# Kernel tuning notes

Hardware: AMD Instinct MI355X
Metric: run time of the kernel (lower is better)

The kernel has to match this reference:

```python
import math
import jax, jax.numpy as jnp
from jax import lax
import numpy as np

THETA = 10.0      # spiking threshold
TAU_SR = 10.0     # SRM (psp) alpha-kernel time constant
TAU_REF = 1.0     # refractory alpha-kernel time constant
SCALE_REF = 2.0   # refractory scale (kernel = -scaleRef*theta*alpha)
TAU_RHO = 1.0     # surrogate-gradient width
TS = 1.0          # simulation time step


def _alpha_filter_scan(x, tau, extra_input_fn=None):
    """Causal convolution along last (time) axis with alpha kernel
    k[n] = (n*Ts/tau) * exp(1 - n*Ts/tau)  (k[0] = 0),
    implemented exactly as a 2-state linear recurrence.
    x: [N, C, T] -> out: [N, C, T]."""
    d = jnp.float32(math.exp(-TS / tau))
    c = jnp.float32(math.e * TS / tau)
    xT = jnp.moveaxis(x, -1, 0)  # [T, N, C]

    def step(carry, xt):
        p, a = carry
        a = d * (a + p)          # alpha response from inputs up to t-1
        p = d * p + xt           # pure exponential state
        return (p, a), a * c

    z = jnp.zeros_like(xT[0])
    _, out = lax.scan(step, (z, z), xT)
    return jnp.moveaxis(out, 0, -1)


def psp(x):
    return _alpha_filter_scan(x, TAU_SR)


@jax.custom_vjp
def spike_fn(v):
    # Heaviside threshold on (membrane - theta)
    return (v >= 0).astype(v.dtype)

def _spike_fwd(v):
    return spike_fn(v), v

def _spike_bwd(v, g):
    # SLAYER surrogate gradient: exponential pdf around threshold
    grad = (1.0 / TAU_RHO) * jnp.exp(-jnp.abs(v) / TAU_RHO)
    return (g * grad,)

spike_fn.defvjp(_spike_fwd, _spike_bwd)


def spike_layer(u_in):
    """Threshold-and-refract over time. u_in: [N, C, T] psp potentials.
    Refractory response = -scaleRef*theta * alpha_{tauRef}(past spikes)."""
    d = jnp.float32(math.exp(-TS / TAU_REF))
    c = jnp.float32(math.e * TS / TAU_REF)
    ref_scale = jnp.float32(-SCALE_REF * THETA)
    uT = jnp.moveaxis(u_in, -1, 0)  # [T, N, C]

    def step(carry, ut):
        p, a = carry
        a = d * (a + p)                      # refractory potential at t
        u = ut + c * a                       # membrane potential
        s = spike_fn(u - THETA)              # spikes (0/1)
        p = d * p + ref_scale * s            # inject refractory impulse
        return (p, a), s

    z = jnp.zeros_like(uT[0])
    _, s = lax.scan(step, (z, z), uT)
    return jnp.moveaxis(s, 0, -1)


def setup_inputs() -> dict:
    key = jax.random.key(0)
    k1, k2, k3 = jax.random.split(key, 3)
    N, I, H, O, T = 64, 256, 1024, 18, 500
    # Bernoulli(0.1) input spikes
    spike_input = (jax.random.uniform(k1, (N, I, T)) < 0.1).astype(jnp.float32)
    W1 = jax.random.normal(k2, (H, I), dtype=jnp.float32) * (1.0 / math.sqrt(I))
    W2 = jax.random.normal(k3, (O, H), dtype=jnp.float32) * (1.0 / math.sqrt(H))
    return {"spike_input": spike_input, "W1": W1, "W2": W2}


def reference(spike_input, W1, W2):
    # layer 1: dense (per-timestep linear) -> psp -> spike
    y1 = jnp.einsum('nit,hi->nht', spike_input, W1)
    s1 = spike_layer(psp(y1))
    # layer 2
    y2 = jnp.einsum('nht,oh->not', s1, W2)
    s2 = spike_layer(psp(y2))
    return s2
```

## Files before the change

### kernel.cpp

```cpp
#include <hip/hip_runtime.h>


#define NN 64
#define II 256
#define HH 1024
#define OO 18
#define TT 500

#define D_SR 0.9048374180359595f
#define C_SR 0.27182818284590454f
#define D_RF 0.36787944117144233f
#define C_RF 2.718281828459045f
#define THETA 10.0f
#define REFS (-20.0f)

typedef _Float16 f16;
typedef _Float16 f16x8 __attribute__((ext_vector_type(8)));
typedef float f32x4 __attribute__((ext_vector_type(4)));

__device__ __forceinline__ void gl2lds16(const void* g, void* l) {
    __builtin_amdgcn_global_load_lds(
        (const __attribute__((address_space(1))) void*)g,
        (__attribute__((address_space(3))) void*)l, 16, 0, 0);
}

__launch_bounds__(256)
__global__ void prep_all(const float* __restrict__ X, const float* __restrict__ W1,
                         const float* __restrict__ W2, f16* __restrict__ Xb,
                         f16* __restrict__ W1h, f16* __restrict__ W1l,
                         f16* __restrict__ W2h, f16* __restrict__ W2l) {
    __shared__ float tile[64][65];
    const int b = blockIdx.x;
    const int tid = threadIdx.x;

    if (b < 2048) {
        const int t0 = (b & 7) * 64, i0 = ((b >> 3) & 3) * 64, n = b >> 5;
        const int tx = tid & 63, q = tid >> 6;
        const float* Xn = X + (size_t)n * II * TT;
#pragma unroll 4
        for (int j = 0; j < 16; ++j) {
            int il = j * 4 + q;
            int t = t0 + tx;
            tile[il][tx] = (t < TT) ? Xn[(size_t)(i0 + il) * TT + t] : 0.f;
        }
        __syncthreads();
#pragma unroll 4
        for (int j = 0; j < 16; ++j) {
            int tl = j * 4 + q;
            int t = t0 + tl;
            if (t < TT)
                Xb[((size_t)n * TT + t) * II + i0 + tx] = (f16)tile[tx][tl];
        }
    } else if (b < 3072) {
        int idx = (b - 2048) * 256 + tid;
        float w = W1[idx];
        f16 h = (f16)w;
        f16 l = (f16)(w - (float)h);
        W1h[idx] = h;
        W1l[idx] = l;
    } else {
        int idx = (b - 3072) * 256 + tid;
        int o = idx >> 10;
        float w = (o < OO) ? W2[idx] : 0.f;
        f16 h = (f16)w;
        f16 l = (f16)(w - (float)h);
        W2h[idx] = h;
        W2l[idx] = l;
    }
}

__launch_bounds__(512)
__global__ void gemm1_scan1(const f16* __restrict__ Xb, const f16* __restrict__ Wh,
                            const f16* __restrict__ Wl, f16* __restrict__ S1) {
    __shared__ __align__(16) char smem[128 * 132 * 4];
    float* yb = (float*)smem;

    const int tid = threadIdx.x;
    const int wave = tid >> 6, lane = tid & 63;

    const int f = blockIdx.y * 8 + blockIdx.x;
    const int x = f & 7, g = f >> 3;
    const int n = x * 8 + (g & 7);
    const int ht = g >> 3;
    const int h0g = ht * 128;

    const int rbl = wave * 16 + (lane >> 2);
    const int koff = (lane & 3) * 8;
    const f16* gBh0 = Wh + (size_t)(h0g + rbl) * II + koff;
    const f16* gBl0 = Wl + (size_t)(h0g + rbl) * II + koff;

    const int wm = wave & 1, wn = wave >> 1;
    const int fr = lane & 15, kq = lane >> 4;

    float p1 = 0.f, a1 = 0.f, p2 = 0.f, a2 = 0.f;

    for (int c = 0; c < 4; ++c) {
        const int t0 = c * 128;
        const int TCe = (TT - t0 < 128) ? (TT - t0) : 128;

        int r0 = rbl; if (r0 > TCe - 1) r0 = TCe - 1;
        const f16* gA0 = Xb + ((size_t)n * TT + t0 + r0) * II + koff;

        auto stage = [&](int kk2, int b) {
            f16* As_b = (f16*)(smem + b * 24576);
            f16* Bh_b = As_b + 4096;
            f16* Bl_b = As_b + 8192;
            const int ko = kk2 * 32;
            gl2lds16(gA0 + ko, As_b + wave * 512);
            gl2lds16(gBh0 + ko, Bh_b + wave * 512);
            gl2lds16(gBl0 + ko, Bl_b + wave * 512);
        };

        stage(0, 0);

        f32x4 acc[4][2] = {};
        for (int kk = 0; kk < 8; ++kk) {
            __syncthreads();
            if (kk < 7) stage(kk + 1, (kk + 1) & 1);

            const f16* As_b = (const f16*)(smem + (kk & 1) * 24576);
            const f16* Bh_b = As_b + 4096;
            const f16* Bl_b = As_b + 8192;

            f16x8 av[4], bhv[2], blv[2];
#pragma unroll
            for (int i = 0; i < 4; ++i)
                av[i] = *(const f16x8*)(As_b + (wm * 64 + i * 16 + fr) * 32 + kq * 8);
#pragma unroll
            for (int j = 0; j < 2; ++j) {
                bhv[j] = *(const f16x8*)(Bh_b + (wn * 32 + j * 16 + fr) * 32 + kq * 8);
                blv[j] = *(const f16x8*)(Bl_b + (wn * 32 + j * 16 + fr) * 32 + kq * 8);
            }
#pragma unroll
            for (int i = 0; i < 4; ++i)
#pragma unroll
                for (int j = 0; j < 2; ++j) {
                    acc[i][j] = __builtin_amdgcn_mfma_f32_16x16x32_f16(av[i], bhv[j], acc[i][j], 0, 0, 0);
                    acc[i][j] = __builtin_amdgcn_mfma_f32_16x16x32_f16(av[i], blv[j], acc[i][j], 0, 0, 0);
                }
        }
        __syncthreads();

#pragma unroll
        for (int i = 0; i < 4; ++i)
#pragma unroll
            for (int j = 0; j < 2; ++j) {
                int tr = wm * 64 + i * 16 + kq * 4;
                int hc = wn * 32 + j * 16 + fr;
#pragma unroll
                for (int r = 0; r < 4; ++r)
                    yb[(tr + r) * 132 + hc] = acc[i][j][r];
            }
        __syncthreads();

        if (tid < 128) {
            f16* sq = S1 + ((size_t)n * TT + t0) * HH + h0g + tid;
            float rb_[8];
#pragma unroll
            for (int j = 0; j < 8; ++j) rb_[j] = yb[j * 132 + tid];
            int t = 0;
            for (; t + 8 <= TCe; t += 8) {
#pragma unroll
                for (int j = 0; j < 8; ++j) {
                    float xv = rb_[j];
                    int tn = t + j + 8;
                    rb_[j] = (tn < TCe) ? yb[tn * 132 + tid] : 0.f;
                    a1 = D_SR * (a1 + p1);
                    p1 = D_SR * p1 + xv;
                    float ut = C_SR * a1;
                    a2 = D_RF * (a2 + p2);
                    float u = ut + C_RF * a2;
                    float s = (u >= THETA) ? 1.0f : 0.0f;
                    p2 = D_RF * p2 + REFS * s;
                    sq[(size_t)(t + j) * HH] = (f16)s;
                }
            }
            int rem = TCe - t;
#pragma unroll
            for (int j = 0; j < 8; ++j) {
                if (j < rem) {
                    float xv = rb_[j];
                    a1 = D_SR * (a1 + p1);
                    p1 = D_SR * p1 + xv;
                    float ut = C_SR * a1;
                    a2 = D_RF * (a2 + p2);
                    float u = ut + C_RF * a2;
                    float s = (u >= THETA) ? 1.0f : 0.0f;
                    p2 = D_RF * p2 + REFS * s;
                    sq[(size_t)(t + j) * HH] = (f16)s;
                }
            }
        }
        __syncthreads();
    }
}

__launch_bounds__(256)
__global__ void gemm2_mfma(const f16* __restrict__ S1, const f16* __restrict__ W2h,
                           const f16* __restrict__ W2l, float* __restrict__ Y2) {
    __shared__ __align__(16) f16 As[2][64 * 32];
    __shared__ __align__(16) f16 Bh[2][32 * 32];
    __shared__ __align__(16) f16 Bl[2][32 * 32];

    const int tid = threadIdx.x;
    const int wave = tid >> 6, lane = tid & 63;
    const int m0 = blockIdx.x * 64;
    const int fr = lane & 15, kq = lane >> 4;

    const f16* gA = S1 + (size_t)(m0 + wave * 16 + (lane >> 2)) * HH + (lane & 3) * 8;
    const f16* gB = (wave < 2 ? W2h : W2l) + (size_t)((wave & 1) * 16 + (lane >> 2)) * HH + (lane & 3) * 8;

    auto stage = [&](int kk2, int b) {
        const int ko = kk2 * 32;
        gl2lds16(gA + ko, &As[b][wave * 512]);
        gl2lds16(gB + ko, (wave < 2 ? &Bh[b][0] : &Bl[b][0]) + (wave & 1) * 512);
    };

    stage(0, 0);

    f32x4 acc[2] = {};
    for (int kk = 0; kk < HH / 32; ++kk) {
        __syncthreads();
        if (kk < HH / 32 - 1) stage(kk + 1, (kk + 1) & 1);
        const int b = kk & 1;

        f16x8 a, bh[2], bl[2];
        a = *(const f16x8*)(&As[b][(wave * 16 + fr) * 32 + kq * 8]);
#pragma unroll
        for (int j = 0; j < 2; ++j) {
            bh[j] = *(const f16x8*)(&Bh[b][(j * 16 + fr) * 32 + kq * 8]);
            bl[j] = *(const f16x8*)(&Bl[b][(j * 16 + fr) * 32 + kq * 8]);
        }
#pragma unroll
        for (int j = 0; j < 2; ++j) {
            acc[j] = __builtin_amdgcn_mfma_f32_16x16x32_f16(a, bh[j], acc[j], 0, 0, 0);
            acc[j] = __builtin_amdgcn_mfma_f32_16x16x32_f16(a, bl[j], acc[j], 0, 0, 0);
        }
    }

#pragma unroll
    for (int j = 0; j < 2; ++j) {
        int rbase = m0 + wave * 16 + kq * 4;
        int cc = j * 16 + fr;
        float* p = Y2 + (size_t)rbase * 32 + cc;
#pragma unroll
        for (int r = 0; r < 4; ++r)
            p[(size_t)r * 32] = acc[j][r];
    }
}

__launch_bounds__(256)
__global__ void scan2_k(const float* __restrict__ Y2, float* __restrict__ Out) {
    __shared__ float yc[TT * 32];
    __shared__ float sb[OO * TT];
    const int n = blockIdx.x, tid = threadIdx.x;

    const float4* src = (const float4*)(Y2 + (size_t)n * TT * 32);
    float4* dst = (float4*)yc;
    for (int i = tid; i < TT * 8; i += 256) dst[i] = src[i];
    __syncthreads();

    if (tid < 32) {
        float p1 = 0.f, a1 = 0.f, p2 = 0.f, a2 = 0.f;
        float rb_[8];
#pragma unroll
        for (int j = 0; j < 8; ++j) rb_[j] = yc[j * 32 + tid];
        int t = 0;
        for (; t + 8 <= TT; t += 8) {
#pragma unroll
            for (int j = 0; j < 8; ++j) {
                float xv = rb_[j];
                int tn = t + j + 8;
                rb_[j] = (tn < TT) ? yc[tn * 32 + tid] : 0.f;
                a1 = D_SR * (a1 + p1);
                p1 = D_SR * p1 + xv;
                float ut = C_SR * a1;
                a2 = D_RF * (a2 + p2);
                float u = ut + C_RF * a2;
                float s = (u >= THETA) ? 1.0f : 0.0f;
                p2 = D_RF * p2 + REFS * s;
                if (tid < OO) sb[tid * TT + t + j] = s;
            }
        }
#pragma unroll
        for (int j = 0; j < 8; ++j) {
            if (t + j < TT) {
                float xv = rb_[j];
                a1 = D_SR * (a1 + p1);
                p1 = D_SR * p1 + xv;
                float ut = C_SR * a1;
                a2 = D_RF * (a2 + p2);
                float u = ut + C_RF * a2;
                float s = (u >= THETA) ? 1.0f : 0.0f;
                p2 = D_RF * p2 + REFS * s;
                if (tid < OO) sb[tid * TT + t + j] = s;
            }
        }
    }
    __syncthreads();

    float* on = Out + (size_t)n * OO * TT;
    for (int e = tid; e < OO * TT; e += 256) on[e] = sb[e];
}

extern "C" void kernel_launch(void* const* d_in, const int* in_sizes, int n_in,
                              void* d_out, int out_size, void* d_ws, size_t ws_size,
                              hipStream_t stream) {
    const float* X  = (const float*)d_in[0];
    const float* W1 = (const float*)d_in[1];
    const float* W2 = (const float*)d_in[2];
    float* out = (float*)d_out;

    const size_t s_s1 = (size_t)NN * TT * HH * 2;
    const size_t s_Xb = (size_t)NN * TT * II * 2;
    const size_t s_W  = (size_t)HH * II * 2;
    const size_t s_W2 = (size_t)32 * HH * 2;

    char* w = (char*)d_ws;
    f16*   s1b = (f16*)w;  w += s_s1;
    f16*   Xb  = (f16*)w;  w += s_Xb;
    f16*   W1h = (f16*)w;  w += s_W;
    f16*   W1l = (f16*)w;  w += s_W;
    f16*   W2h = (f16*)w;  w += s_W2;
    f16*   W2l = (f16*)w;  w += s_W2;
    float* y2  = (float*)w;

    prep_all<<<3200, 256, 0, stream>>>(X, W1, W2, Xb, W1h, W1l, W2h, W2l);

    gemm1_scan1<<<dim3(8, NN), 512, 0, stream>>>(Xb, W1h, W1l, s1b);

    gemm2_mfma<<<(NN * TT) / 64, 256, 0, stream>>>(s1b, W2h, W2l, y2);
    scan2_k<<<NN, 256, 0, stream>>>(y2, out);
}
```

Measured before the change: 188.2 us.

## Triple-buffer LDS staging with vmcnt waits, XOR swizzle, and MFMA priority

```diff
diff --git a/kernel.cpp b/kernel.cpp
--- a/kernel.cpp
+++ b/kernel.cpp
@@ -72,7 +72,7 @@
 __launch_bounds__(512)
 __global__ void gemm1_scan1(const f16* __restrict__ Xb, const f16* __restrict__ Wh,
                             const f16* __restrict__ Wl, f16* __restrict__ S1) {
-    __shared__ __align__(16) char smem[128 * 132 * 4];
+    __shared__ __align__(16) char smem[3 * 24576];
     float* yb = (float*)smem;
 
     const int tid = threadIdx.x;
@@ -85,12 +85,13 @@
     const int h0g = ht * 128;
 
     const int rbl = wave * 16 + (lane >> 2);
-    const int koff = (lane & 3) * 8;
+    const int koff = (((lane & 3) ^ ((lane >> 3) & 3))) * 8;
     const f16* gBh0 = Wh + (size_t)(h0g + rbl) * II + koff;
     const f16* gBl0 = Wl + (size_t)(h0g + rbl) * II + koff;
 
     const int wm = wave & 1, wn = wave >> 1;
     const int fr = lane & 15, kq = lane >> 4;
+    const int kz = (kq ^ ((fr >> 1) & 3)) * 8;
 
     float p1 = 0.f, a1 = 0.f, p2 = 0.f, a2 = 0.f;
 
@@ -112,25 +113,31 @@
         };
 
         stage(0, 0);
+        stage(1, 1);
 
         f32x4 acc[4][2] = {};
+#pragma unroll
         for (int kk = 0; kk < 8; ++kk) {
-            __syncthreads();
-            if (kk < 7) stage(kk + 1, (kk + 1) & 1);
-
-            const f16* As_b = (const f16*)(smem + (kk & 1) * 24576);
+            if (kk < 7) asm volatile("s_waitcnt vmcnt(3)" ::: "memory");
+            else        asm volatile("s_waitcnt vmcnt(0)" ::: "memory");
+            __builtin_amdgcn_s_barrier();
+            __builtin_amdgcn_sched_barrier(0);
+            if (kk < 6) stage(kk + 2, (kk + 2) % 3);
+
+            const f16* As_b = (const f16*)(smem + (kk % 3) * 24576);
             const f16* Bh_b = As_b + 4096;
             const f16* Bl_b = As_b + 8192;
 
             f16x8 av[4], bhv[2], blv[2];
 #pragma unroll
             for (int i = 0; i < 4; ++i)
-                av[i] = *(const f16x8*)(As_b + (wm * 64 + i * 16 + fr) * 32 + kq * 8);
+                av[i] = *(const f16x8*)(As_b + (wm * 64 + i * 16 + fr) * 32 + kz);
 #pragma unroll
             for (int j = 0; j < 2; ++j) {
-                bhv[j] = *(const f16x8*)(Bh_b + (wn * 32 + j * 16 + fr) * 32 + kq * 8);
-                blv[j] = *(const f16x8*)(Bl_b + (wn * 32 + j * 16 + fr) * 32 + kq * 8);
-            }
+                bhv[j] = *(const f16x8*)(Bh_b + (wn * 32 + j * 16 + fr) * 32 + kz);
+                blv[j] = *(const f16x8*)(Bl_b + (wn * 32 + j * 16 + fr) * 32 + kz);
+            }
+            __builtin_amdgcn_s_setprio(1);
 #pragma unroll
             for (int i = 0; i < 4; ++i)
 #pragma unroll
@@ -138,6 +145,7 @@
                     acc[i][j] = __builtin_amdgcn_mfma_f32_16x16x32_f16(av[i], bhv[j], acc[i][j], 0, 0, 0);
                     acc[i][j] = __builtin_amdgcn_mfma_f32_16x16x32_f16(av[i], blv[j], acc[i][j], 0, 0, 0);
                 }
+            __builtin_amdgcn_s_setprio(0);
         }
         __syncthreads();
 
@@ -198,17 +206,19 @@
 __launch_bounds__(256)
 __global__ void gemm2_mfma(const f16* __restrict__ S1, const f16* __restrict__ W2h,
                            const f16* __restrict__ W2l, float* __restrict__ Y2) {
-    __shared__ __align__(16) f16 As[2][64 * 32];
-    __shared__ __align__(16) f16 Bh[2][32 * 32];
-    __shared__ __align__(16) f16 Bl[2][32 * 32];
+    __shared__ __align__(16) f16 As[3][64 * 32];
+    __shared__ __align__(16) f16 Bh[3][32 * 32];
+    __shared__ __align__(16) f16 Bl[3][32 * 32];
 
     const int tid = threadIdx.x;
     const int wave = tid >> 6, lane = tid & 63;
     const int m0 = blockIdx.x * 64;
     const int fr = lane & 15, kq = lane >> 4;
-
-    const f16* gA = S1 + (size_t)(m0 + wave * 16 + (lane >> 2)) * HH + (lane & 3) * 8;
-    const f16* gB = (wave < 2 ? W2h : W2l) + (size_t)((wave & 1) * 16 + (lane >> 2)) * HH + (lane & 3) * 8;
+    const int koff = (((lane & 3) ^ ((lane >> 3) & 3))) * 8;
+    const int kz = (kq ^ ((fr >> 1) & 3)) * 8;
+
+    const f16* gA = S1 + (size_t)(m0 + wave * 16 + (lane >> 2)) * HH + koff;
+    const f16* gB = (wave < 2 ? W2h : W2l) + (size_t)((wave & 1) * 16 + (lane >> 2)) * HH + koff;
 
     auto stage = [&](int kk2, int b) {
         const int ko = kk2 * 32;
@@ -217,25 +227,32 @@
     };
 
     stage(0, 0);
+    stage(1, 1);
 
     f32x4 acc[2] = {};
+#pragma unroll
     for (int kk = 0; kk < HH / 32; ++kk) {
-        __syncthreads();
-        if (kk < HH / 32 - 1) stage(kk + 1, (kk + 1) & 1);
-        const int b = kk & 1;
+        if (kk < HH / 32 - 1) asm volatile("s_waitcnt vmcnt(2)" ::: "memory");
+        else                  asm volatile("s_waitcnt vmcnt(0)" ::: "memory");
+        __builtin_amdgcn_s_barrier();
+        __builtin_amdgcn_sched_barrier(0);
+        if (kk < HH / 32 - 2) stage(kk + 2, (kk + 2) % 3);
+        const int b = kk % 3;
 
         f16x8 a, bh[2], bl[2];
-        a = *(const f16x8*)(&As[b][(wave * 16 + fr) * 32 + kq * 8]);
+        a = *(const f16x8*)(&As[b][(wave * 16 + fr) * 32 + kz]);
 #pragma unroll
         for (int j = 0; j < 2; ++j) {
-            bh[j] = *(const f16x8*)(&Bh[b][(j * 16 + fr) * 32 + kq * 8]);
-            bl[j] = *(const f16x8*)(&Bl[b][(j * 16 + fr) * 32 + kq * 8]);
-        }
+            bh[j] = *(const f16x8*)(&Bh[b][(j * 16 + fr) * 32 + kz]);
+            bl[j] = *(const f16x8*)(&Bl[b][(j * 16 + fr) * 32 + kz]);
+        }
+        __builtin_amdgcn_s_setprio(1);
 #pragma unroll
         for (int j = 0; j < 2; ++j) {
             acc[j] = __builtin_amdgcn_mfma_f32_16x16x32_f16(a, bh[j], acc[j], 0, 0, 0);
             acc[j] = __builtin_amdgcn_mfma_f32_16x16x32_f16(a, bl[j], acc[j], 0, 0, 0);
         }
+        __builtin_amdgcn_s_setprio(0);
     }
 
 #pragma unroll
```

Result: no change. 187.4 us (-0.4%).

## Load MFMA operands directly from global memory instead of staging through LDS

Applied to the files above, without the earlier changes.

```diff
diff --git a/kernel.cpp b/kernel.cpp
--- a/kernel.cpp
+++ b/kernel.cpp
@@ -17,12 +17,6 @@
 typedef _Float16 f16;
 typedef _Float16 f16x8 __attribute__((ext_vector_type(8)));
 typedef float f32x4 __attribute__((ext_vector_type(4)));
-
-__device__ __forceinline__ void gl2lds16(const void* g, void* l) {
-    __builtin_amdgcn_global_load_lds(
-        (const __attribute__((address_space(1))) void*)g,
-        (__attribute__((address_space(3))) void*)l, 16, 0, 0);
-}
 
 __launch_bounds__(256)
 __global__ void prep_all(const float* __restrict__ X, const float* __restrict__ W1,
@@ -69,11 +63,10 @@
     }
 }
 
-__launch_bounds__(512)
+__launch_bounds__(512, 4)
 __global__ void gemm1_scan1(const f16* __restrict__ Xb, const f16* __restrict__ Wh,
                             const f16* __restrict__ Wl, f16* __restrict__ S1) {
-    __shared__ __align__(16) char smem[128 * 132 * 4];
-    float* yb = (float*)smem;
+    __shared__ float yb[128 * 132];
 
     const int tid = threadIdx.x;
     const int wave = tid >> 6, lane = tid & 63;
@@ -84,13 +77,12 @@
     const int ht = g >> 3;
     const int h0g = ht * 128;
 
-    const int rbl = wave * 16 + (lane >> 2);
-    const int koff = (lane & 3) * 8;
-    const f16* gBh0 = Wh + (size_t)(h0g + rbl) * II + koff;
-    const f16* gBl0 = Wl + (size_t)(h0g + rbl) * II + koff;
-
     const int wm = wave & 1, wn = wave >> 1;
     const int fr = lane & 15, kq = lane >> 4;
+
+    const f16* gA = Xb + (size_t)n * TT * II;
+    size_t bo0 = (size_t)(h0g + wn * 32 + fr) * II + kq * 8;
+    size_t bo1 = bo0 + (size_t)16 * II;
 
     float p1 = 0.f, a1 = 0.f, p2 = 0.f, a2 = 0.f;
 
@@ -98,47 +90,35 @@
         const int t0 = c * 128;
         const int TCe = (TT - t0 < 128) ? (TT - t0) : 128;
 
-        int r0 = rbl; if (r0 > TCe - 1) r0 = TCe - 1;
-        const f16* gA0 = Xb + ((size_t)n * TT + t0 + r0) * II + koff;
-
-        auto stage = [&](int kk2, int b) {
-            f16* As_b = (f16*)(smem + b * 24576);
-            f16* Bh_b = As_b + 4096;
-            f16* Bl_b = As_b + 8192;
-            const int ko = kk2 * 32;
-            gl2lds16(gA0 + ko, As_b + wave * 512);
-            gl2lds16(gBh0 + ko, Bh_b + wave * 512);
-            gl2lds16(gBl0 + ko, Bl_b + wave * 512);
-        };
-
-        stage(0, 0);
+        size_t ao[4];
+#pragma unroll
+        for (int i = 0; i < 4; ++i) {
+            int r = t0 + wm * 64 + i * 16 + fr;
+            if (r > TT - 1) r = TT - 1;
+            ao[i] = (size_t)r * II + kq * 8;
+        }
 
         f32x4 acc[4][2] = {};
+#pragma unroll
         for (int kk = 0; kk < 8; ++kk) {
-            __syncthreads();
-            if (kk < 7) stage(kk + 1, (kk + 1) & 1);
-
-            const f16* As_b = (const f16*)(smem + (kk & 1) * 24576);
-            const f16* Bh_b = As_b + 4096;
-            const f16* Bl_b = As_b + 8192;
-
-            f16x8 av[4], bhv[2], blv[2];
+            const int ko = kk * 32;
+            f16x8 av[4], bh[2], bl[2];
 #pragma unroll
             for (int i = 0; i < 4; ++i)
-                av[i] = *(const f16x8*)(As_b + (wm * 64 + i * 16 + fr) * 32 + kq * 8);
-#pragma unroll
-            for (int j = 0; j < 2; ++j) {
-                bhv[j] = *(const f16x8*)(Bh_b + (wn * 32 + j * 16 + fr) * 32 + kq * 8);
-                blv[j] = *(const f16x8*)(Bl_b + (wn * 32 + j * 16 + fr) * 32 + kq * 8);
-            }
+                av[i] = *(const f16x8*)(gA + ao[i] + ko);
+            bh[0] = *(const f16x8*)(Wh + bo0 + ko);
+            bh[1] = *(const f16x8*)(Wh + bo1 + ko);
+            bl[0] = *(const f16x8*)(Wl + bo0 + ko);
+            bl[1] = *(const f16x8*)(Wl + bo1 + ko);
 #pragma unroll
             for (int i = 0; i < 4; ++i)
 #pragma unroll
                 for (int j = 0; j < 2; ++j) {
-                    acc[i][j] = __builtin_amdgcn_mfma_f32_16x16x32_f16(av[i], bhv[j], acc[i][j], 0, 0, 0);
-                    acc[i][j] = __builtin_amdgcn_mfma_f32_16x16x32_f16(av[i], blv[j], acc[i][j], 0, 0, 0);
+                    acc[i][j] = __builtin_amdgcn_mfma_f32_16x16x32_f16(av[i], bh[j], acc[i][j], 0, 0, 0);
+                    acc[i][j] = __builtin_amdgcn_mfma_f32_16x16x32_f16(av[i], bl[j], acc[i][j], 0, 0, 0);
                 }
         }
+
         __syncthreads();
 
 #pragma unroll
@@ -191,46 +171,31 @@
                 }
             }
         }
-        __syncthreads();
     }
 }
 
 __launch_bounds__(256)
 __global__ void gemm2_mfma(const f16* __restrict__ S1, const f16* __restrict__ W2h,
                            const f16* __restrict__ W2l, float* __restrict__ Y2) {
-    __shared__ __align__(16) f16 As[2][64 * 32];
-    __shared__ __align__(16) f16 Bh[2][32 * 32];
-    __shared__ __align__(16) f16 Bl[2][32 * 32];
-
     const int tid = threadIdx.x;
     const int wave = tid >> 6, lane = tid & 63;
     const int m0 = blockIdx.x * 64;
     const int fr = lane & 15, kq = lane >> 4;
 
-    const f16* gA = S1 + (size_t)(m0 + wave * 16 + (lane >> 2)) * HH + (lane & 3) * 8;
-    const f16* gB = (wave < 2 ? W2h : W2l) + (size_t)((wave & 1) * 16 + (lane >> 2)) * HH + (lane & 3) * 8;
-
-    auto stage = [&](int kk2, int b) {
-        const int ko = kk2 * 32;
-        gl2lds16(gA + ko, &As[b][wave * 512]);
-        gl2lds16(gB + ko, (wave < 2 ? &Bh[b][0] : &Bl[b][0]) + (wave & 1) * 512);
-    };
-
-    stage(0, 0);
+    const f16* gA = S1 + (size_t)(m0 + wave * 16 + fr) * HH + kq * 8;
+    size_t bo0 = (size_t)fr * HH + kq * 8;
+    size_t bo1 = bo0 + (size_t)16 * HH;
 
     f32x4 acc[2] = {};
+#pragma unroll 8
     for (int kk = 0; kk < HH / 32; ++kk) {
-        __syncthreads();
-        if (kk < HH / 32 - 1) stage(kk + 1, (kk + 1) & 1);
-        const int b = kk & 1;
-
+        const int ko = kk * 32;
         f16x8 a, bh[2], bl[2];
-        a = *(const f16x8*)(&As[b][(wave * 16 + fr) * 32 + kq * 8]);
-#pragma unroll
-        for (int j = 0; j < 2; ++j) {
-            bh[j] = *(const f16x8*)(&Bh[b][(j * 16 + fr) * 32 + kq * 8]);
-            bl[j] = *(const f16x8*)(&Bl[b][(j * 16 + fr) * 32 + kq * 8]);
-        }
+        a = *(const f16x8*)(gA + ko);
+        bh[0] = *(const f16x8*)(W2h + bo0 + ko);
+        bh[1] = *(const f16x8*)(W2h + bo1 + ko);
+        bl[0] = *(const f16x8*)(W2l + bo0 + ko);
+        bl[1] = *(const f16x8*)(W2l + bo1 + ko);
 #pragma unroll
         for (int j = 0; j < 2; ++j) {
             acc[j] = __builtin_amdgcn_mfma_f32_16x16x32_f16(a, bh[j], acc[j], 0, 0, 0);
```

New measurement: 280.0 us. 1.49x slower.
